# Optimization experiments

Hardware: AMD Instinct MI355X
Metric: run time of the kernel (lower is better)

The kernel has to match this reference:

```python
import jax, jax.numpy as jnp
import numpy as np

# dims (see shape_source)
B, N, P, H, M, E, HOPS = 512, 102, 12, 256, 4, 3, 2
C_CLIP = 10.0   # logit clipping constant params['C']
T = 1.0         # temperature params['T']
NEG = -1e9


def setup_inputs() -> dict:
    key = jax.random.key(0)
    ks = jax.random.split(key, 18)
    s = 0.08  # uniform init range as in _initialize_weights, use scaled normals
    inp = {
        "node_features": jax.random.normal(ks[0], (B, N, P), jnp.float32),
        "adjacency": jax.random.uniform(ks[1], (B, E, N, N), jnp.float32),  # per-edge-cat weighted adjacency
        "mask": jax.random.randint(ks[2], (B, N), 0, 2).astype(jnp.int32),  # 1 = already scheduled / forbidden
        # encoder params
        "W_emb": jax.random.normal(ks[3], (P, H), jnp.float32) * s,
        "W_rel": jax.random.normal(ks[4], (HOPS, E, H, H), jnp.float32) * s / np.sqrt(H),
        "W_self": jax.random.normal(ks[5], (HOPS, H, H), jnp.float32) * s / np.sqrt(H),
        # multi-head glimpse params (Vec / W_q / W_ref per head)
        "Vec": jax.random.normal(ks[6], (M, H, H), jnp.float32) * s,
        "W_q": jax.random.normal(ks[7], (M, 3 * H, H), jnp.float32) * s,
        "W_ref": jax.random.normal(ks[8], (M, H, H), jnp.float32) * s,
        "W_mh": jax.random.normal(ks[9], (M * H, H), jnp.float32) * s,  # multi_head_embedding
        # final pointer params
        "Vec2": jax.random.normal(ks[10], (H,), jnp.float32) * s,
        "W_q2": jax.random.normal(ks[11], (H, H), jnp.float32) * s,
        "W_ref2": jax.random.normal(ks[12], (H, H), jnp.float32) * s,
        # learned decoder seed vectors
        "dec_input": jax.random.normal(ks[13], (H,), jnp.float32) * s,
        "v_1": jax.random.normal(ks[14], (H,), jnp.float32) * s,
    }
    return inp


def reference(node_features, adjacency, mask, W_emb, W_rel, W_self, Vec, W_q,
              W_ref, W_mh, Vec2, W_q2, W_ref2, dec_input, v_1):
    # ---- encoder: linear embedding + HOPS of relational (per-edge-category) message passing ----
    h = jnp.einsum('bnp,ph->bnh', node_features, W_emb)            # [B,N,H]
    for hop in range(HOPS):
        msg = jnp.einsum('benm,bmh->benh', adjacency, h)           # gather neighbors per edge cat
        h = jax.nn.relu(jnp.einsum('benh,ehk->bnk', msg, W_rel[hop])
                        + jnp.einsum('bnh,hk->bnk', h, W_self[hop]))
    enc = h                                                         # [B,N,H]

    # ---- decoder query: cat(graph readout, learned dec_input, learned v_1) -> 3H ----
    enc_mean = enc.mean(axis=1)                                     # [B,H]
    q_cat = jnp.concatenate([enc_mean,
                             jnp.broadcast_to(dec_input, (B, H)),
                             jnp.broadcast_to(v_1, (B, H))], axis=-1)  # [B,3H]

    # ---- multi-head additive (Bahdanau) glimpse: per-head Vec/W_q/W_ref tanh scoring ----
    q = jnp.einsum('bf,mfh->bmh', q_cat, W_q)                       # [B,M,H]
    r = jnp.einsum('bnh,mhk->bmnk', enc, W_ref)                     # [B,M,N,H]
    u = jnp.einsum('bmnh,mhk->bmnk', jnp.tanh(q[:, :, None, :] + r), Vec)
    scores = u.sum(axis=-1)                                         # [B,M,N]
    scores = jnp.where(mask[:, None, :] > 0, NEG, scores)
    a = jax.nn.softmax(scores, axis=-1)
    ctx = jnp.einsum('bmn,bnh->bmh', a, enc).reshape(B, M * H)
    query2 = ctx @ W_mh                                             # [B,H]

    # ---- final pointer head (Vec2 / W_q2 / W_ref2) ----
    u2 = jnp.einsum('h,bnh->bn', Vec2,
                    jnp.tanh((query2 @ W_q2)[:, None, :] + jnp.einsum('bnh,hk->bnk', enc, W_ref2)))
    u2 = C_CLIP * jnp.tanh(u2)                                      # logit clipping
    u2 = jnp.where(mask > 0, NEG, u2)
    log_p = jax.nn.log_softmax(u2 / T, axis=-1)                     # [B,N]
    return log_p
```

## Files before the change

kernel.cpp:

```cpp
#include <hip/hip_runtime.h>
#include <hip/hip_bf16.h>

#define B 512
#define N 102
#define Pdim 12
#define H 256
#define M 4
#define E 3
#define NEG (-1e9f)
#define RT 52224
#define NN (N * N)

typedef __hip_bfloat16 bf16;
typedef __attribute__((ext_vector_type(8))) short short8;
typedef __attribute__((ext_vector_type(4))) float f32x4;
typedef __attribute__((ext_vector_type(16))) float f32x16;

__device__ __forceinline__ float b2f(bf16 v) { return __bfloat162float(v); }
__device__ __forceinline__ bf16 f2b(float v) { return __float2bfloat16(v); }
__device__ __forceinline__ short f2bs(float v) {
    bf16 t = __float2bfloat16(v);
    return *reinterpret_cast<short*>(&t);
}
__device__ __forceinline__ float fast_tanh(float x) {
    float e = __expf(2.f * x);
    return 1.f - 2.f * __builtin_amdgcn_rcpf(e + 1.f);
}

__global__ __launch_bounds__(256) void wt_prep(const float* __restrict__ Wrel,
                                               const float* __restrict__ Wself,
                                               const float* __restrict__ Wref,
                                               const float* __restrict__ Wref2,
                                               const float* __restrict__ Wmh,
                                               const float* __restrict__ Wq2,
                                               const float* __restrict__ W_q,
                                               const float* __restrict__ Vec,
                                               const float* __restrict__ dec,
                                               const float* __restrict__ v1,
                                               short* __restrict__ wfrag,
                                               short* __restrict__ wrefT,
                                               short* __restrict__ wref2T,
                                               short* __restrict__ wmh_bf,
                                               short* __restrict__ wq2_bf,
                                               short* __restrict__ wq_bf,
                                               float* __restrict__ qconst,
                                               float* __restrict__ vsum) {
    if (blockIdx.x >= 5632) {
        int m = blockIdx.x - 5632, hh = threadIdx.x;
        __shared__ float dls[H], vls[H];
        dls[hh] = dec[hh];
        vls[hh] = v1[hh];
        __syncthreads();
        const float* Wm = W_q + (size_t)m * (3 * H) * H;
        float s = 0.f;
        for (int f = 0; f < H; ++f)
            s += dls[f] * Wm[(H + f) * H + hh] + vls[f] * Wm[(2 * H + f) * H + hh];
        qconst[m * H + hh] = s;
        float vs = 0.f;
        const float* Vr = Vec + ((size_t)m * H + hh) * H;
        for (int k = 0; k < H; ++k) vs += Vr[k];
        vsum[m * H + hh] = vs;
        return;
    }
    int idx = blockIdx.x * 256 + threadIdx.x;
    if (idx < 524288) {
        int j = idx & 7;
        int lq = (idx >> 3) & 63;
        int ks = (idx >> 9) & 31;
        int ct = (idx >> 14) & 15;
        int hop = idx >> 18;
        int c = ct * 16 + (lq & 15);
        int k = ks * 32 + ((lq >> 4) & 3) * 8 + j;
        float v;
        if (k < 768) {
            int e = k >> 8, kk = k & 255;
            v = Wrel[(((size_t)hop * E + e) * H + kk) * H + c];
        } else {
            v = Wself[((size_t)hop * H + (k - 768)) * H + c];
        }
        wfrag[idx] = f2bs(v);
    } else if (idx < 786432) {
        int r = idx - 524288;
        int row = r >> 8, k = r & 255;
        int m = row >> 8, c = row & 255;
        wrefT[r] = f2bs(Wref[((size_t)m * H + k) * H + c]);
    } else if (idx < 851968) {
        int r = idx - 786432;
        int c = r >> 8, k = r & 255;
        wref2T[r] = f2bs(Wref2[k * H + c]);
    } else if (idx < 1114112) {
        int r = idx - 851968;
        wmh_bf[r] = f2bs(Wmh[r]);
    } else if (idx < 1179648) {
        int r = idx - 1114112;
        wq2_bf[r] = f2bs(Wq2[r]);
    } else if (idx < 1441792) {
        int r = idx - 1179648;
        int m = r >> 16, fh = r & 65535;
        wq_bf[r] = f2bs(W_q[(size_t)m * 768 * 256 + fh]);
    }
}

__global__ __launch_bounds__(256) void embed_k(const float* __restrict__ nf,
                                               const float* __restrict__ W_emb,
                                               bf16* __restrict__ h) {
    int r0 = blockIdx.x * 64;
    int tid = threadIdx.x;
    __shared__ float fs[64][Pdim];
    for (int i = tid; i < 64 * Pdim; i += 256)
        fs[i / Pdim][i % Pdim] = nf[(size_t)r0 * Pdim + i];
    float w[Pdim];
#pragma unroll
    for (int p = 0; p < Pdim; ++p) w[p] = W_emb[p * H + tid];
    __syncthreads();
    for (int r = 0; r < 64; ++r) {
        float s = 0.f;
#pragma unroll
        for (int p = 0; p < Pdim; ++p) s += fs[r][p] * w[p];
        h[(size_t)(r0 + r) * H + tid] = f2b(s);
    }
}

#define HP 264
#define YP 136
#define AREG 11
__global__ __launch_bounds__(1024, 4) void hop_fused(const bf16* __restrict__ hin,
                                                     const float* __restrict__ adj,
                                                     const short* __restrict__ wfragp,
                                                     bf16* __restrict__ hout,
                                                     float* __restrict__ mean_out) {
    int b = blockIdx.x;
    int tid = threadIdx.x;
    int w = tid >> 6;
    int l = tid & 63;
    int cg = l & 15;
    int rg = (l >> 4) & 3;

    __shared__ short hS[112 * HP];
    __shared__ short YtS[256 * YP];
    __shared__ short AsS[112 * YP];

    const short8 z8 = {0, 0, 0, 0, 0, 0, 0, 0};
    for (int i = tid; i < (112 * YP) / 8; i += 1024) ((short8*)AsS)[i] = z8;
    for (int i = tid; i < 10 * 32; i += 1024) {
        int n = 102 + (i >> 5), g = i & 31;
        *(short8*)(&hS[n * HP + g * 8]) = z8;
    }
    for (int i = tid; i < 512; i += 1024) {
        int c = i >> 1, part = i & 1;
        *(short8*)(&YtS[c * YP + 112 + part * 8]) = z8;
    }
    const short* hp = (const short*)hin;
    for (int i = tid; i < 102 * 32; i += 1024) {
        int n = i >> 5, g = i & 31;
        *(short8*)(&hS[n * HP + g * 8]) = *(const short8*)(hp + ((size_t)b * N + n) * H + g * 8);
    }

    int offA[AREG];
    bool valA[AREG];
#pragma unroll
    for (int i = 0; i < AREG; ++i) {
        int id = tid + (i << 10);
        valA[i] = (id < NN);
        int n = id / N, m = id - n * N;
        offA[i] = valA[i] ? (n * YP + m) : 0;
    }
    const float* Ab0 = adj + ((size_t)b * E) * NN;
    float areg[AREG];
#pragma unroll
    for (int i = 0; i < AREG; ++i) {
        int id = tid + (i << 10);
        areg[i] = valA[i] ? Ab0[id] : 0.f;
    }
    __syncthreads();

    const short8* wf8 = (const short8*)wfragp;

    f32x4 hacc[7];
#pragma unroll
    for (int j = 0; j < 7; ++j) hacc[j] = (f32x4){0.f, 0.f, 0.f, 0.f};

    for (int e = 0; e < E; ++e) {
        f32x4 g[7];
#pragma unroll
        for (int j = 0; j < 7; ++j) g[j] = (f32x4){0.f, 0.f, 0.f, 0.f};
#pragma unroll
        for (int ks = 0; ks < 8; ++ks) {
            short8 wfa = wf8[(w * 32 + e * 8 + ks) * 64 + l];
#pragma unroll
            for (int mt = 0; mt < 7; ++mt) {
                short8 hf = *(const short8*)(&hS[(mt * 16 + cg) * HP + ks * 32 + rg * 8]);
                g[mt] = __builtin_amdgcn_mfma_f32_16x16x32_bf16(wfa, hf, g[mt], 0, 0, 0);
            }
        }
#pragma unroll
        for (int i = 0; i < AREG; ++i)
            if (valA[i]) AsS[offA[i]] = f2bs(areg[i]);
        if (e < E - 1) {
            const float* Abn = adj + ((size_t)b * E + e + 1) * NN;
#pragma unroll
            for (int i = 0; i < AREG; ++i) {
                int id = tid + (i << 10);
                if (valA[i]) areg[i] = Abn[id];
            }
        }
#pragma unroll
        for (int mt = 0; mt < 7; ++mt)
#pragma unroll
            for (int r = 0; r < 4; ++r) {
                int c = w * 16 + rg * 4 + r;
                YtS[c * YP + mt * 16 + cg] = f2bs(g[mt][r]);
            }
        __syncthreads();
#pragma unroll
        for (int ks = 0; ks < 4; ++ks) {
            short8 yf = *(const short8*)(&YtS[(w * 16 + cg) * YP + ks * 32 + rg * 8]);
#pragma unroll
            for (int nt = 0; nt < 7; ++nt) {
                short8 af = *(const short8*)(&AsS[(nt * 16 + cg) * YP + ks * 32 + rg * 8]);
                hacc[nt] = __builtin_amdgcn_mfma_f32_16x16x32_bf16(af, yf, hacc[nt], 0, 0, 0);
            }
        }
        __syncthreads();
    }
#pragma unroll
    for (int ks = 0; ks < 8; ++ks) {
        short8 wfa = wf8[(w * 32 + 24 + ks) * 64 + l];
#pragma unroll
        for (int nt = 0; nt < 7; ++nt) {
            short8 hf = *(const short8*)(&hS[(nt * 16 + cg) * HP + ks * 32 + rg * 8]);
            hacc[nt] = __builtin_amdgcn_mfma_f32_16x16x32_bf16(hf, wfa, hacc[nt], 0, 0, 0);
        }
    }
    __syncthreads();
#pragma unroll
    for (int nt = 0; nt < 7; ++nt)
#pragma unroll
        for (int r = 0; r < 4; ++r) {
            int n = nt * 16 + rg * 4 + r;
            int c = w * 16 + cg;
            float v = hacc[nt][r];
            hS[n * HP + c] = f2bs(v > 0.f ? v : 0.f);
        }
    __syncthreads();
    short* ho = (short*)hout;
    for (int i = tid; i < 102 * 32; i += 1024) {
        int n = i >> 5, g = i & 31;
        *(short8*)(ho + ((size_t)b * N + n) * H + g * 8) = *(const short8*)(&hS[n * HP + g * 8]);
    }
    if (mean_out) {
        float* partf = (float*)AsS;
        int c = tid & 255, qq = tid >> 8;
        float s = 0.f;
        for (int n = qq; n < N; n += 4) s += b2f(*(const bf16*)&hS[n * HP + c]);
        partf[qq * 256 + c] = s;
        __syncthreads();
        if (tid < 256)
            mean_out[(size_t)b * H + tid] =
                (partf[tid] + partf[256 + tid] + partf[512 + tid] + partf[768 + tid]) * (1.f / (float)N);
    }
}

__global__ __launch_bounds__(256, 2) void head2_mfma(const bf16* __restrict__ X,
                                                     const short* __restrict__ WT,
                                                     const float* __restrict__ qb, int qbs,
                                                     const float* __restrict__ vsb,
                                                     float* __restrict__ outp, int obs) {
    int rt = blockIdx.x, m = blockIdx.y;
    int r0 = rt * 128;
    int tid = threadIdx.x;
    int w = tid >> 6, l = tid & 63;
    int lr = l & 31;
    int lh = l >> 5;
    __shared__ short Xs[128 * 256];
    __shared__ float qls[3 * 256];
    __shared__ float part[4][128];

    const short* Xp = (const short*)X;
#pragma unroll
    for (int i = 0; i < 16; ++i) {
        int id = tid + i * 256;
        int r = id >> 5, g = id & 31;
        short8 v = *(const short8*)(Xp + (size_t)(r0 + r) * H + g * 8);
        *(short8*)((char*)Xs + r * 512 + ((g ^ (r & 7)) * 16)) = v;
    }
    int b_base = r0 / N;
#pragma unroll
    for (int i = 0; i < 3; ++i) {
        int bb = b_base + i;
        if (bb > B - 1) bb = B - 1;
        qls[i * 256 + tid] = qb[(size_t)bb * qbs + m * H + tid];
    }
    const short8* w8 = (const short8*)WT;
    int cbase = m * 256 + w * 64;
    short8 afr0[16], afr1[16];
#pragma unroll
    for (int ks = 0; ks < 16; ++ks) {
        afr0[ks] = w8[(size_t)(cbase + lr) * 32 + ks * 2 + lh];
        afr1[ks] = w8[(size_t)(cbase + 32 + lr) * 32 + ks * 2 + lh];
    }
    float vsl[32];
#pragma unroll
    for (int j = 0; j < 16; ++j) {
        int cl = (j & 3) + 8 * (j >> 2) + 4 * lh;
        vsl[j]      = vsb[m * H + w * 64 + cl];
        vsl[16 + j] = vsb[m * H + w * 64 + 32 + cl];
    }
    __syncthreads();

    int swz = lr & 7;
    for (int t = 0; t < 4; ++t) {
        f32x16 acc0, acc1;
#pragma unroll
        for (int j = 0; j < 16; ++j) { acc0[j] = 0.f; acc1[j] = 0.f; }
        const char* xbase = (const char*)Xs + (t * 32 + lr) * 512;
#pragma unroll
        for (int ks = 0; ks < 16; ++ks) {
            short8 bx = *(const short8*)(xbase + (((2 * ks + lh) ^ swz) * 16));
            acc0 = __builtin_amdgcn_mfma_f32_32x32x16_bf16(afr0[ks], bx, acc0, 0, 0, 0);
            acc1 = __builtin_amdgcn_mfma_f32_32x32x16_bf16(afr1[ks], bx, acc1, 0, 0, 0);
        }
        int r = r0 + t * 32 + lr;
        int b = r / N;
        int boff = b - b_base;
        float s = 0.f;
#pragma unroll
        for (int j = 0; j < 16; ++j) {
            int cl = (j & 3) + 8 * (j >> 2) + 4 * lh;
            float x0 = qls[boff * 256 + w * 64 + cl] + acc0[j];
            s += fast_tanh(x0) * vsl[j];
            float x1 = qls[boff * 256 + w * 64 + 32 + cl] + acc1[j];
            s += fast_tanh(x1) * vsl[16 + j];
        }
        s += __shfl_xor(s, 32, 64);
        if (l < 32) part[w][t * 32 + lr] = s;
    }
    __syncthreads();
    if (tid < 128) {
        int r = r0 + tid;
        int b = r / N, n = r - b * N;
        outp[(size_t)b * obs + m * N + n] = part[0][tid] + part[1][tid] + part[2][tid] + part[3][tid];
    }
}

__global__ __launch_bounds__(256) void q_k(const float* __restrict__ enc_mean,
                                           const short* __restrict__ wq_bf,
                                           const float* __restrict__ qconst,
                                           float* __restrict__ qbuf) {
    int bid = blockIdx.x;
    int b = bid >> 2, m = bid & 3;
    int hh = threadIdx.x;
    __shared__ float em[H];
    em[hh] = enc_mean[(size_t)b * H + hh];
    __syncthreads();
    const bf16* Wm = (const bf16*)(wq_bf + (size_t)m * 65536);
    float s = qconst[m * H + hh];
    for (int f = 0; f < H; ++f) s += em[f] * b2f(Wm[f * H + hh]);
    qbuf[((size_t)b * M + m) * H + hh] = s;
}

__global__ __launch_bounds__(256) void softmax_ctx_k(const float* __restrict__ scores,
                                                     const int* __restrict__ mask,
                                                     const bf16* __restrict__ enc,
                                                     float* __restrict__ ctx) {
    int bid = blockIdx.x;
    int b = bid >> 2, m = bid & 3;
    int tid = threadIdx.x;
    __shared__ float a[128];
    __shared__ float red[2];
    float sv = NEG;
    if (tid < N)
        sv = (mask[(size_t)b * N + tid] > 0) ? NEG : scores[((size_t)b * M + m) * N + tid];
    if (tid < 128) a[tid] = sv;
    __syncthreads();
    if (tid < 64) {
        float v = fmaxf(a[tid], a[tid + 64]);
        v = fmaxf(v, __shfl_xor(v, 32, 64));
        v = fmaxf(v, __shfl_xor(v, 16, 64));
        v = fmaxf(v, __shfl_xor(v, 8, 64));
        v = fmaxf(v, __shfl_xor(v, 4, 64));
        v = fmaxf(v, __shfl_xor(v, 2, 64));
        v = fmaxf(v, __shfl_xor(v, 1, 64));
        if (tid == 0) red[0] = v;
    }
    __syncthreads();
    float mx = red[0];
    float ev = (tid < N) ? __expf(sv - mx) : 0.f;
    if (tid < 128) a[tid] = ev;
    __syncthreads();
    if (tid < 64) {
        float v = a[tid] + a[tid + 64];
        v += __shfl_xor(v, 32, 64);
        v += __shfl_xor(v, 16, 64);
        v += __shfl_xor(v, 8, 64);
        v += __shfl_xor(v, 4, 64);
        v += __shfl_xor(v, 2, 64);
        v += __shfl_xor(v, 1, 64);
        if (tid == 0) red[1] = __builtin_amdgcn_rcpf(v);
    }
    __syncthreads();
    float inv = red[1];
    float c = 0.f;
    for (int n = 0; n < N; ++n)
        c += a[n] * b2f(enc[((size_t)b * N + n) * H + tid]);
    ctx[((size_t)b * M + m) * H + tid] = c * inv;
}

__global__ __launch_bounds__(256) void query2_k(const float* __restrict__ ctx,
                                                const short* __restrict__ wmh,
                                                const short* __restrict__ wq2,
                                                float* __restrict__ q2) {
    int b = blockIdx.x;
    int tid = threadIdx.x;
    __shared__ float cx[M * H];
    __shared__ float qy[H];
    for (int idx = tid; idx < M * H; idx += 256) cx[idx] = ctx[(size_t)b * M * H + idx];
    __syncthreads();
    const bf16* wm = (const bf16*)wmh;
    float acc = 0.f;
    for (int j = 0; j < M * H; ++j) acc += cx[j] * b2f(wm[(size_t)j * H + tid]);
    qy[tid] = acc;
    __syncthreads();
    const bf16* w2 = (const bf16*)wq2;
    float acc2 = 0.f;
    for (int k = 0; k < H; ++k) acc2 += qy[k] * b2f(w2[(size_t)k * H + tid]);
    q2[(size_t)b * H + tid] = acc2;
}

__global__ __launch_bounds__(128) void final_out_k(const float* __restrict__ u2,
                                                   const int* __restrict__ mask,
                                                   float* __restrict__ out) {
    int b = blockIdx.x;
    int tid = threadIdx.x;
    __shared__ float a[128];
    __shared__ float red[2];
    float u = NEG;
    if (tid < N) {
        u = 10.f * fast_tanh(u2[(size_t)b * N + tid]);
        if (mask[(size_t)b * N + tid] > 0) u = NEG;
    }
    a[tid] = u;
    __syncthreads();
    if (tid < 64) {
        float v = fmaxf(a[tid], a[tid + 64]);
        v = fmaxf(v, __shfl_xor(v, 32, 64));
        v = fmaxf(v, __shfl_xor(v, 16, 64));
        v = fmaxf(v, __shfl_xor(v, 8, 64));
        v = fmaxf(v, __shfl_xor(v, 4, 64));
        v = fmaxf(v, __shfl_xor(v, 2, 64));
        v = fmaxf(v, __shfl_xor(v, 1, 64));
        if (tid == 0) red[0] = v;
    }
    __syncthreads();
    float mx = red[0];
    float ev = (tid < N) ? __expf(u - mx) : 0.f;
    a[tid] = ev;
    __syncthreads();
    if (tid < 64) {
        float v = a[tid] + a[tid + 64];
        v += __shfl_xor(v, 32, 64);
        v += __shfl_xor(v, 16, 64);
        v += __shfl_xor(v, 8, 64);
        v += __shfl_xor(v, 4, 64);
        v += __shfl_xor(v, 2, 64);
        v += __shfl_xor(v, 1, 64);
        if (tid == 0) red[1] = logf(v);
    }
    __syncthreads();
    if (tid < N) out[(size_t)b * N + tid] = (u - mx) - red[1];
}

extern "C" void kernel_launch(void* const* d_in, const int* in_sizes, int n_in,
                              void* d_out, int out_size, void* d_ws, size_t ws_size,
                              hipStream_t stream) {
    const float* nf     = (const float*)d_in[0];
    const float* adj    = (const float*)d_in[1];
    const int*   mask   = (const int*)d_in[2];
    const float* W_emb  = (const float*)d_in[3];
    const float* W_rel  = (const float*)d_in[4];
    const float* W_self = (const float*)d_in[5];
    const float* Vec    = (const float*)d_in[6];
    const float* W_q    = (const float*)d_in[7];
    const float* W_ref  = (const float*)d_in[8];
    const float* W_mh   = (const float*)d_in[9];
    const float* Vec2   = (const float*)d_in[10];
    const float* W_q2   = (const float*)d_in[11];
    const float* W_ref2 = (const float*)d_in[12];
    const float* dec    = (const float*)d_in[13];
    const float* v_1    = (const float*)d_in[14];
    float* out = (float*)d_out;

    char* p = (char*)d_ws;
    size_t off = 0;
    auto alloc = [&](size_t bytes) -> char* {
        char* q = p + off;
        off += (bytes + 255) & ~(size_t)255;
        return q;
    };
    bf16* hA    = (bf16*)alloc((size_t)RT * H * sizeof(bf16));
    bf16* hB    = (bf16*)alloc((size_t)RT * H * sizeof(bf16));
    short* wfrag  = (short*)alloc(524288 * sizeof(short));
    short* wrefT  = (short*)alloc(262144 * sizeof(short));
    short* wref2T = (short*)alloc(65536 * sizeof(short));
    short* wmh_bf = (short*)alloc(262144 * sizeof(short));
    short* wq2_bf = (short*)alloc(65536 * sizeof(short));
    short* wq_bf  = (short*)alloc(262144 * sizeof(short));
    float* enc_mean = (float*)alloc((size_t)B * H * sizeof(float));
    float* qconst   = (float*)alloc((size_t)M * H * sizeof(float));
    float* vsumb    = (float*)alloc((size_t)M * H * sizeof(float));
    float* qbuf     = (float*)alloc((size_t)B * M * H * sizeof(float));
    float* scoresb  = (float*)alloc((size_t)B * M * N * sizeof(float));
    float* ctxb     = (float*)alloc((size_t)B * M * H * sizeof(float));
    float* q2b      = (float*)alloc((size_t)B * H * sizeof(float));
    float* u2b      = (float*)alloc((size_t)B * N * sizeof(float));

    wt_prep<<<5636, 256, 0, stream>>>(W_rel, W_self, W_ref, W_ref2, W_mh, W_q2,
                                      W_q, Vec, dec, v_1,
                                      wfrag, wrefT, wref2T, wmh_bf, wq2_bf, wq_bf,
                                      qconst, vsumb);
    embed_k<<<RT / 64, 256, 0, stream>>>(nf, W_emb, hA);

    hop_fused<<<B, 1024, 0, stream>>>(hA, adj, wfrag, hB, nullptr);
    hop_fused<<<B, 1024, 0, stream>>>(hB, adj, wfrag + 262144, hA, enc_mean);

    const bf16* enc = hA;

    q_k<<<B * M, 256, 0, stream>>>(enc_mean, wq_bf, qconst, qbuf);
    head2_mfma<<<dim3(RT / 128, M), 256, 0, stream>>>(enc, wrefT, qbuf, M * H, vsumb, scoresb, M * N);
    softmax_ctx_k<<<B * M, 256, 0, stream>>>(scoresb, mask, enc, ctxb);
    query2_k<<<B, 256, 0, stream>>>(ctxb, wmh_bf, wq2_bf, q2b);
    head2_mfma<<<dim3(RT / 128, 1), 256, 0, stream>>>(enc, wref2T, q2b, H, Vec2, u2b, N);
    final_out_k<<<B, 128, 0, stream>>>(u2b, mask, out);
}
```

Before: 293.5 us.

## Fuse embedding into first hop, halve hop block size, transpose weight prep via LDS

The separate embedding kernel is removed. The first hop kernel now computes the node embedding in-block with MFMA, using a new bf16 fragment of W_emb that weight prep builds. The hop kernel drops from 1024 to 512 threads per block, with each wave handling two column tiles. The adjacency for edge 0 is staged into LDS up front, the self-term MFMA moves ahead of the relational loop, and the Y tile uses a swizzled per-wave layout to cut LDS bank conflicts. Weight-fragment prep now goes through a shared-memory transpose so global reads are coalesced, at the cost of extra syncs and higher register pressure per thread.

```diff
diff --git a/kernel.cpp b/kernel.cpp
--- a/kernel.cpp
+++ b/kernel.cpp
@@ -9,7 +9,7 @@
 #define E 3
 #define NEG (-1e9f)
 #define RT 52224
-#define NN (N * N)
+#define NN 10404
 
 typedef __hip_bfloat16 bf16;
 typedef __attribute__((ext_vector_type(8))) short short8;
@@ -35,6 +35,7 @@
                                                const float* __restrict__ Wq2,
                                                const float* __restrict__ W_q,
                                                const float* __restrict__ Vec,
+                                               const float* __restrict__ W_emb,
                                                const float* __restrict__ dec,
                                                const float* __restrict__ v1,
                                                short* __restrict__ wfrag,
@@ -43,10 +44,36 @@
                                                short* __restrict__ wmh_bf,
                                                short* __restrict__ wq2_bf,
                                                short* __restrict__ wq_bf,
+                                               short* __restrict__ wembf,
                                                float* __restrict__ qconst,
                                                float* __restrict__ vsum) {
-    if (blockIdx.x >= 5632) {
-        int m = blockIdx.x - 5632, hh = threadIdx.x;
+    int bid = blockIdx.x;
+    int tid = threadIdx.x;
+    __shared__ short tl[1024 * 17];
+    if (bid < 32) {
+        int hop = bid >> 4, ct = bid & 15;
+        for (int i = tid; i < 16384; i += 256) {
+            int k = i >> 4, c0 = i & 15;
+            int c = ct * 16 + c0;
+            float v;
+            if (k < 768) v = Wrel[(((size_t)hop * E + (k >> 8)) * H + (k & 255)) * H + c];
+            else         v = Wself[((size_t)hop * H + (k - 768)) * H + c];
+            tl[k * 17 + c0] = f2bs(v);
+        }
+        __syncthreads();
+        short8* outp = (short8*)wfrag + (size_t)(hop * 16 + ct) * 2048;
+        for (int i = tid; i < 2048; i += 256) {
+            int ks = i >> 6, lq = i & 63;
+            int c0 = lq & 15, kb = (lq >> 4) * 8;
+            short8 v;
+#pragma unroll
+            for (int j = 0; j < 8; ++j) v[j] = tl[(ks * 32 + kb + j) * 17 + c0];
+            outp[i] = v;
+        }
+        return;
+    }
+    if (bid >= 3648) {
+        int m = bid - 3648, hh = tid;
         __shared__ float dls[H], vls[H];
         dls[hh] = dec[hh];
         vls[hh] = v1[hh];
@@ -62,24 +89,8 @@
         vsum[m * H + hh] = vs;
         return;
     }
-    int idx = blockIdx.x * 256 + threadIdx.x;
-    if (idx < 524288) {
-        int j = idx & 7;
-        int lq = (idx >> 3) & 63;
-        int ks = (idx >> 9) & 31;
-        int ct = (idx >> 14) & 15;
-        int hop = idx >> 18;
-        int c = ct * 16 + (lq & 15);
-        int k = ks * 32 + ((lq >> 4) & 3) * 8 + j;
-        float v;
-        if (k < 768) {
-            int e = k >> 8, kk = k & 255;
-            v = Wrel[(((size_t)hop * E + e) * H + kk) * H + c];
-        } else {
-            v = Wself[((size_t)hop * H + (k - 768)) * H + c];
-        }
-        wfrag[idx] = f2bs(v);
-    } else if (idx < 786432) {
+    int idx = 524288 + (bid - 32) * 256 + tid;
+    if (idx < 786432) {
         int r = idx - 524288;
         int row = r >> 8, k = r & 255;
         int m = row >> 8, c = row & 255;
@@ -98,138 +109,188 @@
         int r = idx - 1179648;
         int m = r >> 16, fh = r & 65535;
         wq_bf[r] = f2bs(W_q[(size_t)m * 768 * 256 + fh]);
-    }
-}
-
-__global__ __launch_bounds__(256) void embed_k(const float* __restrict__ nf,
-                                               const float* __restrict__ W_emb,
-                                               bf16* __restrict__ h) {
-    int r0 = blockIdx.x * 64;
-    int tid = threadIdx.x;
-    __shared__ float fs[64][Pdim];
-    for (int i = tid; i < 64 * Pdim; i += 256)
-        fs[i / Pdim][i % Pdim] = nf[(size_t)r0 * Pdim + i];
-    float w[Pdim];
-#pragma unroll
-    for (int p = 0; p < Pdim; ++p) w[p] = W_emb[p * H + tid];
-    __syncthreads();
-    for (int r = 0; r < 64; ++r) {
-        float s = 0.f;
-#pragma unroll
-        for (int p = 0; p < Pdim; ++p) s += fs[r][p] * w[p];
-        h[(size_t)(r0 + r) * H + tid] = f2b(s);
+    } else if (idx < 1449984) {
+        int r = idx - 1441792;
+        int ct = r >> 9, lq = (r >> 3) & 63, j = r & 7;
+        int c = ct * 16 + (lq & 15), k = (lq >> 4) * 8 + j;
+        wembf[r] = (k < Pdim) ? f2bs(W_emb[k * H + c]) : (short)0;
     }
 }
 
 #define HP 264
-#define YP 136
-#define AREG 11
-__global__ __launch_bounds__(1024, 4) void hop_fused(const bf16* __restrict__ hin,
-                                                     const float* __restrict__ adj,
-                                                     const short* __restrict__ wfragp,
-                                                     bf16* __restrict__ hout,
-                                                     float* __restrict__ mean_out) {
+#define YTP 136
+#define ASP 136
+#define AITER 21
+__global__ __launch_bounds__(512, 2) void hop_fused(const bf16* __restrict__ hin,
+                                                    const float* __restrict__ nf,
+                                                    const short* __restrict__ wembf,
+                                                    const float* __restrict__ adj,
+                                                    const short* __restrict__ wfragp,
+                                                    bf16* __restrict__ hout,
+                                                    float* __restrict__ mean_out) {
     int b = blockIdx.x;
     int tid = threadIdx.x;
     int w = tid >> 6;
     int l = tid & 63;
     int cg = l & 15;
-    int rg = (l >> 4) & 3;
+    int rg = l >> 4;
+    int ct0 = 2 * w, ct1 = 2 * w + 1;
 
     __shared__ short hS[112 * HP];
-    __shared__ short YtS[256 * YP];
-    __shared__ short AsS[112 * YP];
+    __shared__ short YtS[8 * 32 * YTP];
+    __shared__ short AsS[112 * ASP];
 
     const short8 z8 = {0, 0, 0, 0, 0, 0, 0, 0};
-    for (int i = tid; i < (112 * YP) / 8; i += 1024) ((short8*)AsS)[i] = z8;
-    for (int i = tid; i < 10 * 32; i += 1024) {
+    for (int i = tid; i < (8 * 32 * YTP) / 8; i += 512) ((short8*)YtS)[i] = z8;
+    for (int i = tid; i < 10 * 32; i += 512) {
         int n = 102 + (i >> 5), g = i & 31;
         *(short8*)(&hS[n * HP + g * 8]) = z8;
     }
-    for (int i = tid; i < 512; i += 1024) {
-        int c = i >> 1, part = i & 1;
-        *(short8*)(&YtS[c * YP + 112 + part * 8]) = z8;
-    }
-    const short* hp = (const short*)hin;
-    for (int i = tid; i < 102 * 32; i += 1024) {
-        int n = i >> 5, g = i & 31;
-        *(short8*)(&hS[n * HP + g * 8]) = *(const short8*)(hp + ((size_t)b * N + n) * H + g * 8);
-    }
-
-    int offA[AREG];
-    bool valA[AREG];
-#pragma unroll
-    for (int i = 0; i < AREG; ++i) {
-        int id = tid + (i << 10);
-        valA[i] = (id < NN);
-        int n = id / N, m = id - n * N;
-        offA[i] = valA[i] ? (n * YP + m) : 0;
-    }
-    const float* Ab0 = adj + ((size_t)b * E) * NN;
-    float areg[AREG];
-#pragma unroll
-    for (int i = 0; i < AREG; ++i) {
-        int id = tid + (i << 10);
-        areg[i] = valA[i] ? Ab0[id] : 0.f;
+    for (int i = tid; i < 112 * 26; i += 512) {
+        int n = i / 26, m = 102 + (i % 26);
+        AsS[n * ASP + m] = 0;
+    }
+    for (int i = tid; i < 10 * 102; i += 512) {
+        int n = 102 + i / 102, m = i % 102;
+        AsS[n * ASP + m] = 0;
+    }
+    int offA[AITER];
+    {
+        const float* Ab0 = adj + (size_t)b * E * NN;
+#pragma unroll
+        for (int i = 0; i < AITER; ++i) {
+            int id = tid + (i << 9);
+            if (id < NN) {
+                int n = id / N, m = id - n * N;
+                offA[i] = n * ASP + m;
+                AsS[offA[i]] = f2bs(Ab0[id]);
+            } else offA[i] = -1;
+        }
+    }
+    float areg[AITER];
+    {
+        const float* Ab1 = adj + ((size_t)b * E + 1) * NN;
+#pragma unroll
+        for (int i = 0; i < AITER; ++i) {
+            int id = tid + (i << 9);
+            areg[i] = (id < NN) ? Ab1[id] : 0.f;
+        }
+    }
+    if (hin) {
+        const short* hp = (const short*)hin;
+        for (int i = tid; i < 102 * 32; i += 512) {
+            int n = i >> 5, g = i & 31;
+            *(short8*)(&hS[n * HP + g * 8]) = *(const short8*)(hp + ((size_t)b * N + n) * H + g * 8);
+        }
+    } else {
+        const short8* we8 = (const short8*)wembf;
+        short8 bf0 = we8[ct0 * 64 + l];
+        short8 bf1 = we8[ct1 * 64 + l];
+#pragma unroll
+        for (int nt = 0; nt < 7; ++nt) {
+            int row = nt * 16 + cg;
+            short8 afr = z8;
+            if (row < 102 && rg < 2) {
+                const float* src = nf + ((size_t)b * N + row) * Pdim + rg * 8;
+                f32x4 v0 = *(const f32x4*)src;
+                afr[0] = f2bs(v0[0]); afr[1] = f2bs(v0[1]);
+                afr[2] = f2bs(v0[2]); afr[3] = f2bs(v0[3]);
+                if (rg == 0) {
+                    f32x4 v1 = *(const f32x4*)(src + 4);
+                    afr[4] = f2bs(v1[0]); afr[5] = f2bs(v1[1]);
+                    afr[6] = f2bs(v1[2]); afr[7] = f2bs(v1[3]);
+                }
+            }
+            f32x4 d0 = (f32x4){0.f, 0.f, 0.f, 0.f}, d1 = d0;
+            d0 = __builtin_amdgcn_mfma_f32_16x16x32_bf16(afr, bf0, d0, 0, 0, 0);
+            d1 = __builtin_amdgcn_mfma_f32_16x16x32_bf16(afr, bf1, d1, 0, 0, 0);
+#pragma unroll
+            for (int r = 0; r < 4; ++r) {
+                int n = nt * 16 + rg * 4 + r;
+                hS[n * HP + ct0 * 16 + cg] = f2bs(d0[r]);
+                hS[n * HP + ct1 * 16 + cg] = f2bs(d1[r]);
+            }
+        }
     }
     __syncthreads();
 
     const short8* wf8 = (const short8*)wfragp;
-
-    f32x4 hacc[7];
-#pragma unroll
-    for (int j = 0; j < 7; ++j) hacc[j] = (f32x4){0.f, 0.f, 0.f, 0.f};
-
+    f32x4 hacc0[7], hacc1[7];
+#pragma unroll
+    for (int j = 0; j < 7; ++j) {
+        hacc0[j] = (f32x4){0.f, 0.f, 0.f, 0.f};
+        hacc1[j] = hacc0[j];
+    }
+
+#pragma unroll
+    for (int ks = 0; ks < 8; ++ks) {
+        short8 wfs0 = wf8[(ct0 * 32 + 24 + ks) * 64 + l];
+        short8 wfs1 = wf8[(ct1 * 32 + 24 + ks) * 64 + l];
+#pragma unroll
+        for (int nt = 0; nt < 7; ++nt) {
+            short8 hf = *(const short8*)(&hS[(nt * 16 + cg) * HP + ks * 32 + rg * 8]);
+            hacc0[nt] = __builtin_amdgcn_mfma_f32_16x16x32_bf16(hf, wfs0, hacc0[nt], 0, 0, 0);
+            hacc1[nt] = __builtin_amdgcn_mfma_f32_16x16x32_bf16(hf, wfs1, hacc1[nt], 0, 0, 0);
+        }
+    }
+
+    int ytbase = w * (32 * YTP);
     for (int e = 0; e < E; ++e) {
-        f32x4 g[7];
-#pragma unroll
-        for (int j = 0; j < 7; ++j) g[j] = (f32x4){0.f, 0.f, 0.f, 0.f};
+        if (e > 0) {
+            __syncthreads();
+#pragma unroll
+            for (int i = 0; i < AITER; ++i)
+                if (offA[i] >= 0) AsS[offA[i]] = f2bs(areg[i]);
+            if (e < E - 1) {
+                const float* Abn = adj + ((size_t)b * E + e + 1) * NN;
+#pragma unroll
+                for (int i = 0; i < AITER; ++i) {
+                    int id = tid + (i << 9);
+                    if (id < NN) areg[i] = Abn[id];
+                }
+            }
+            __syncthreads();
+        }
+        f32x4 g0[7], g1[7];
+#pragma unroll
+        for (int j = 0; j < 7; ++j) {
+            g0[j] = (f32x4){0.f, 0.f, 0.f, 0.f};
+            g1[j] = g0[j];
+        }
 #pragma unroll
         for (int ks = 0; ks < 8; ++ks) {
-            short8 wfa = wf8[(w * 32 + e * 8 + ks) * 64 + l];
+            short8 wfa0 = wf8[(ct0 * 32 + e * 8 + ks) * 64 + l];
+            short8 wfa1 = wf8[(ct1 * 32 + e * 8 + ks) * 64 + l];
 #pragma unroll
             for (int mt = 0; mt < 7; ++mt) {
                 short8 hf = *(const short8*)(&hS[(mt * 16 + cg) * HP + ks * 32 + rg * 8]);
-                g[mt] = __builtin_amdgcn_mfma_f32_16x16x32_bf16(wfa, hf, g[mt], 0, 0, 0);
+                g0[mt] = __builtin_amdgcn_mfma_f32_16x16x32_bf16(wfa0, hf, g0[mt], 0, 0, 0);
+                g1[mt] = __builtin_amdgcn_mfma_f32_16x16x32_bf16(wfa1, hf, g1[mt], 0, 0, 0);
             }
         }
 #pragma unroll
-        for (int i = 0; i < AREG; ++i)
-            if (valA[i]) AsS[offA[i]] = f2bs(areg[i]);
-        if (e < E - 1) {
-            const float* Abn = adj + ((size_t)b * E + e + 1) * NN;
-#pragma unroll
-            for (int i = 0; i < AREG; ++i) {
-                int id = tid + (i << 10);
-                if (valA[i]) areg[i] = Abn[id];
+        for (int mt = 0; mt < 7; ++mt) {
+            int gl = mt * 2 + (cg >> 3);
+            int gp0 = ((gl + rg) & 15) * 8 + (cg & 7);
+            int gp1 = ((gl + 4 + rg) & 15) * 8 + (cg & 7);
+#pragma unroll
+            for (int r = 0; r < 4; ++r) {
+                YtS[ytbase + (rg * 4 + r) * YTP + gp0] = f2bs(g0[mt][r]);
+                YtS[ytbase + (16 + rg * 4 + r) * YTP + gp1] = f2bs(g1[mt][r]);
             }
         }
 #pragma unroll
-        for (int mt = 0; mt < 7; ++mt)
-#pragma unroll
-            for (int r = 0; r < 4; ++r) {
-                int c = w * 16 + rg * 4 + r;
-                YtS[c * YP + mt * 16 + cg] = f2bs(g[mt][r]);
+        for (int ks = 0; ks < 4; ++ks) {
+            short8 yf0 = *(const short8*)(&YtS[ytbase + cg * YTP +
+                                               (((ks * 4 + rg) + (cg >> 2)) & 15) * 8]);
+            short8 yf1 = *(const short8*)(&YtS[ytbase + (16 + cg) * YTP +
+                                               (((ks * 4 + rg) + 4 + (cg >> 2)) & 15) * 8]);
+#pragma unroll
+            for (int nt = 0; nt < 7; ++nt) {
+                short8 af = *(const short8*)(&AsS[(nt * 16 + cg) * ASP + ks * 32 + rg * 8]);
+                hacc0[nt] = __builtin_amdgcn_mfma_f32_16x16x32_bf16(af, yf0, hacc0[nt], 0, 0, 0);
+                hacc1[nt] = __builtin_amdgcn_mfma_f32_16x16x32_bf16(af, yf1, hacc1[nt], 0, 0, 0);
             }
-        __syncthreads();
-#pragma unroll
-        for (int ks = 0; ks < 4; ++ks) {
-            short8 yf = *(const short8*)(&YtS[(w * 16 + cg) * YP + ks * 32 + rg * 8]);
-#pragma unroll
-            for (int nt = 0; nt < 7; ++nt) {
-                short8 af = *(const short8*)(&AsS[(nt * 16 + cg) * YP + ks * 32 + rg * 8]);
-                hacc[nt] = __builtin_amdgcn_mfma_f32_16x16x32_bf16(af, yf, hacc[nt], 0, 0, 0);
-            }
-        }
-        __syncthreads();
-    }
-#pragma unroll
-    for (int ks = 0; ks < 8; ++ks) {
-        short8 wfa = wf8[(w * 32 + 24 + ks) * 64 + l];
-#pragma unroll
-        for (int nt = 0; nt < 7; ++nt) {
-            short8 hf = *(const short8*)(&hS[(nt * 16 + cg) * HP + ks * 32 + rg * 8]);
-            hacc[nt] = __builtin_amdgcn_mfma_f32_16x16x32_bf16(hf, wfa, hacc[nt], 0, 0, 0);
         }
     }
     __syncthreads();
@@ -238,13 +299,13 @@
 #pragma unroll
         for (int r = 0; r < 4; ++r) {
             int n = nt * 16 + rg * 4 + r;
-            int c = w * 16 + cg;
-            float v = hacc[nt][r];
-            hS[n * HP + c] = f2bs(v > 0.f ? v : 0.f);
+            float v0 = hacc0[nt][r], v1 = hacc1[nt][r];
+            hS[n * HP + ct0 * 16 + cg] = f2bs(v0 > 0.f ? v0 : 0.f);
+            hS[n * HP + ct1 * 16 + cg] = f2bs(v1 > 0.f ? v1 : 0.f);
         }
     __syncthreads();
     short* ho = (short*)hout;
-    for (int i = tid; i < 102 * 32; i += 1024) {
+    for (int i = tid; i < 102 * 32; i += 512) {
         int n = i >> 5, g = i & 31;
         *(short8*)(ho + ((size_t)b * N + n) * H + g * 8) = *(const short8*)(&hS[n * HP + g * 8]);
     }
@@ -252,12 +313,12 @@
         float* partf = (float*)AsS;
         int c = tid & 255, qq = tid >> 8;
         float s = 0.f;
-        for (int n = qq; n < N; n += 4) s += b2f(*(const bf16*)&hS[n * HP + c]);
+        for (int n = qq; n < N; n += 2) s += b2f(*(const bf16*)&hS[n * HP + c]);
         partf[qq * 256 + c] = s;
         __syncthreads();
         if (tid < 256)
             mean_out[(size_t)b * H + tid] =
-                (partf[tid] + partf[256 + tid] + partf[512 + tid] + partf[768 + tid]) * (1.f / (float)N);
+                (partf[tid] + partf[256 + tid]) * (1.f / (float)N);
     }
 }
 
@@ -505,6 +566,7 @@
     short* wmh_bf = (short*)alloc(262144 * sizeof(short));
     short* wq2_bf = (short*)alloc(65536 * sizeof(short));
     short* wq_bf  = (short*)alloc(262144 * sizeof(short));
+    short* wembf  = (short*)alloc(8192 * sizeof(short));
     float* enc_mean = (float*)alloc((size_t)B * H * sizeof(float));
     float* qconst   = (float*)alloc((size_t)M * H * sizeof(float));
     float* vsumb    = (float*)alloc((size_t)M * H * sizeof(float));
@@ -514,14 +576,13 @@
     float* q2b      = (float*)alloc((size_t)B * H * sizeof(float));
     float* u2b      = (float*)alloc((size_t)B * N * sizeof(float));
 
-    wt_prep<<<5636, 256, 0, stream>>>(W_rel, W_self, W_ref, W_ref2, W_mh, W_q2,
-                                      W_q, Vec, dec, v_1,
-                                      wfrag, wrefT, wref2T, wmh_bf, wq2_bf, wq_bf,
+    wt_prep<<<3652, 256, 0, stream>>>(W_rel, W_self, W_ref, W_ref2, W_mh, W_q2,
+                                      W_q, Vec, W_emb, dec, v_1,
+                                      wfrag, wrefT, wref2T, wmh_bf, wq2_bf, wq_bf, wembf,
                                       qconst, vsumb);
-    embed_k<<<RT / 64, 256, 0, stream>>>(nf, W_emb, hA);
-
-    hop_fused<<<B, 1024, 0, stream>>>(hA, adj, wfrag, hB, nullptr);
-    hop_fused<<<B, 1024, 0, stream>>>(hB, adj, wfrag + 262144, hA, enc_mean);
+
+    hop_fused<<<B, 512, 0, stream>>>(nullptr, nf, wembf, adj, wfrag, hB, nullptr);
+    hop_fused<<<B, 512, 0, stream>>>(hB, nullptr, wembf, adj, wfrag + 262144, hA, enc_mean);
 
     const bf16* enc = hA;
 
```

After: 331.4 us. +12.9%, slower.
